# Performance work log

Measured on AMD Instinct MI355X. Metric: run time of the kernel, lower is better.

The kernel has to match this reference:

```python
import jax, jax.numpy as jnp
import numpy as np

G = 9.8          # gravity constant from the module
B = 1024         # buckets per mid layer == spigots per bucket
M = 14           # number of homogeneous mid layers
L = M + 2        # total network layers (head bucket + mids + outlet layer)


def _solve_bucket(H0, S_b, theta_b, inflow):
    """Faithful port of solve_single_bucket.
    H0: scalar head, S_b: (n_sp, 2) [spigot height, area], theta_b: (n_sp,),
    inflow: scalar. Sequential spigot loop -> lax.scan.
    Note: after the first spigot, H_effective = H0 - cum_q/2 (inflow dropped),
    exactly as in the torch code."""
    def step(carry, x):
        H_eff, cum = carry
        sp_h, sp_a, th = x
        h = jnp.maximum(0.0, H_eff - sp_h)
        q = th * jnp.sqrt(2.0 * G * h) * sp_a
        cum = cum + q
        return (H0 - 0.5 * cum, cum), q
    init = (H0 + inflow, jnp.zeros((), S_b.dtype))
    (_, cum_q), qs = jax.lax.scan(step, init, (S_b[:, 0], S_b[:, 1], theta_b))
    H_final = H0 - cum_q + inflow
    return H_final, qs


def setup_inputs() -> dict:
    key = jax.random.key(0)
    ks = jax.random.split(key, 10)
    H0 = jax.random.uniform(ks[0], (1,), jnp.float32) * 5.0
    H_mid = jax.random.uniform(ks[1], (M, B), jnp.float32) * 5.0
    H_last = jax.random.uniform(ks[2], (B,), jnp.float32) * 5.0
    S0 = jax.random.uniform(ks[3], (1, B, 2), jnp.float32)
    S_mid = jax.random.uniform(ks[4], (M, B, B, 2), jnp.float32)
    S_last = jax.random.uniform(ks[5], (B, 1, 2), jnp.float32)
    theta0 = jax.random.uniform(ks[6], (B,), jnp.float32)
    theta_mid = jax.random.uniform(ks[7], (M, B, B), jnp.float32)
    theta_last = jax.random.uniform(ks[8], (B,), jnp.float32)
    precip = jax.random.uniform(ks[9], (), jnp.float32) * 2.0
    return {"H0": H0, "H_mid": H_mid, "H_last": H_last,
            "S0": S0, "S_mid": S_mid, "S_last": S_last,
            "theta0": theta0, "theta_mid": theta_mid, "theta_last": theta_last,
            "precip": precip}


def reference(H0, H_mid, H_last, S0, S_mid, S_last, theta0, theta_mid, theta_last, precip):
    p_layer = precip / L            # precip_inflow_per_layer ('even')
    p_bucket = p_layer / B          # per-bucket share in B-bucket layers

    # layer 0: single head bucket with B spigots, inflow = precip/L
    H0_new, q0 = _solve_bucket(H0[0], S0[0], theta0, p_layer)
    inflow = q0 + p_bucket          # inflow to each of layer-1's B buckets

    # mid layers: vmap over buckets, scan over layers (sequential dependency)
    def mid_layer(inflow, xs):
        H_l, S_l, th_l = xs         # (B,), (B,B,2), (B,B)
        Hn, q = jax.vmap(_solve_bucket)(H_l, S_l, th_l, inflow)
        return q.sum(axis=0) + p_bucket, Hn
    inflow, H_mid_new = jax.lax.scan(mid_layer, inflow, (H_mid, S_mid, theta_mid))

    # last layer: B buckets with a single outlet spigot each
    H_last_new, q_last = jax.vmap(_solve_bucket)(H_last, S_last, theta_last[:, None], inflow)

    # flat output: new heads of all layers + outlet flows
    return jnp.concatenate([H0_new[None], H_mid_new.reshape(-1), H_last_new, q_last.reshape(-1)])
```

## Files before the change

kernel.cpp:

```cpp
#include <hip/hip_runtime.h>
#include <math.h>

#define TWO_G 19.6f
#define NBLK  256

__device__ __attribute__((aligned(256))) unsigned g_flags[NBLK];

__device__ __forceinline__ float flow_q(float th, float d, float a) {
    return th * sqrtf(TWO_G * d) * a;
}

__device__ __forceinline__ float wave_sum(float v) {
#pragma unroll
    for (int o = 32; o > 0; o >>= 1) v += __shfl_xor(v, o);
    return v;
}

__device__ __forceinline__ float lane_bcast(float v, int j) {
    return __int_as_float(__builtin_amdgcn_readlane(__float_as_int(v), j));
}

__device__ __forceinline__ float ld_agent(const float* p) {
    return __hip_atomic_load(p, __ATOMIC_RELAXED, __HIP_MEMORY_SCOPE_AGENT);
}
__device__ __forceinline__ void st_agent(float* p, float v) {
    __hip_atomic_store(p, v, __ATOMIC_RELAXED, __HIP_MEMORY_SCOPE_AGENT);
}
__device__ __forceinline__ unsigned ld_flag(const unsigned* p) {
    return __hip_atomic_load(p, __ATOMIC_RELAXED, __HIP_MEMORY_SCOPE_AGENT);
}
__device__ __forceinline__ void st_flag(unsigned* p, unsigned v) {
    __hip_atomic_store(p, v, __ATOMIC_RELAXED, __HIP_MEMORY_SCOPE_AGENT);
}

__device__ __forceinline__ void dma16(const void* g, void* l) {
    __builtin_amdgcn_global_load_lds(
        (const __attribute__((address_space(1))) unsigned int*)g,
        (__attribute__((address_space(3))) unsigned int*)l, 16, 0, 0);
}

__device__ __forceinline__ void grid_barrier(unsigned target, int bid, int tid) {
    __syncthreads();
    if (tid < 64) {
        if (tid == 0) st_flag(&g_flags[bid], target);
        for (;;) {
            int ok = 1;
#pragma unroll
            for (int k = 0; k < 4; ++k) {
                unsigned f = ld_flag(&g_flags[k * 64 + tid]);
                ok &= ((int)(f - target) >= 0);
            }
            if (__all(ok)) break;
            __builtin_amdgcn_s_sleep(1);
        }
    }
    __syncthreads();
    asm volatile("" ::: "memory");
}

__device__ __forceinline__ float solve_lds(float H, float inflow, int lane,
                                           const char* buf, float* acc) {
    const float2* Sb = (const float2*)buf;
    const float*  Tb = (const float*)(buf + 8192);

    float2 s_cur = Sb[lane];
    float  t_cur = Tb[lane];

    float h0 = lane_bcast(s_cur.x, 0);
    float a0 = lane_bcast(s_cur.y, 0);
    float t0 = lane_bcast(t_cur, 0);
    float d0 = (H + inflow) - h0;
    float q0 = (d0 > 0.0f) ? flow_q(t0, d0, a0) : 0.0f;
    float cum = q0;
    float u   = H - 0.5f * cum;
    if (lane == 0 && q0 != 0.0f) atomicAdd(&acc[0], q0);

#pragma unroll
    for (int c = 0; c < 16; ++c) {
        float2 s = s_cur;
        float  t = t_cur;
        if (c < 15) {
            s_cur = Sb[(c + 1) * 64 + lane];
            t_cur = Tb[(c + 1) * 64 + lane];
        }
        unsigned long long avail = (c == 0) ? ~1ull : ~0ull;
        unsigned long long cand  = __ballot(s.x < u) & avail;
        float qmine = 0.0f;
        while (cand) {
            int j = __builtin_ctzll(cand);
            float hj = lane_bcast(s.x, j);
            float aj = lane_bcast(s.y, j);
            float tj = lane_bcast(t, j);
            float d = u - hj;
            float q = flow_q(tj, d, aj);
            cum += q;
            u = H - 0.5f * cum;
            if (lane == j) qmine = q;
            if (j >= 63) break;
            avail &= (~0ull << (j + 1));
            cand = __ballot(s.x < u) & avail;
        }
        if (qmine != 0.0f) atomicAdd(&acc[c * 64 + lane], qmine);
    }
    return cum;
}

__device__ __forceinline__ void layer0_body(const float* __restrict__ H0p,
                                            const float* __restrict__ S0,
                                            const float* __restrict__ theta0,
                                            const float* __restrict__ precip,
                                            float* __restrict__ out,
                                            float* __restrict__ P0, int lane) {
    const float H  = H0p[0];
    const float pl = precip[0] * 0.0625f;
    const float2* S2 = (const float2*)S0;
    float2 sv[16]; float tv[16];
#pragma unroll
    for (int c = 0; c < 16; ++c) { sv[c] = S2[c * 64 + lane]; tv[c] = theta0[c * 64 + lane]; }

    float h0 = lane_bcast(sv[0].x, 0);
    float a0 = lane_bcast(sv[0].y, 0);
    float t0 = lane_bcast(tv[0], 0);
    float d0 = (H + pl) - h0;
    float q0 = (d0 > 0.0f) ? flow_q(t0, d0, a0) : 0.0f;
    float cum = q0;
    float u   = H - 0.5f * cum;
    if (lane == 0) st_agent(&P0[0], q0);

#pragma unroll
    for (int c = 0; c < 16; ++c) {
        int i = c * 64 + lane;
        float2 s = sv[c];
        unsigned long long avail = (c == 0) ? ~1ull : ~0ull;
        unsigned long long cand  = __ballot(s.x < u) & avail;
        float qmine = 0.0f;
        while (cand) {
            int j = __builtin_ctzll(cand);
            float hj = lane_bcast(s.x, j);
            float aj = lane_bcast(s.y, j);
            float tj = lane_bcast(tv[c], j);
            float d = u - hj;
            float q = flow_q(tj, d, aj);
            cum += q;
            u = H - 0.5f * cum;
            if (lane == j) qmine = q;
            if (j >= 63) break;
            avail &= (~0ull << (j + 1));
            cand = __ballot(s.x < u) & avail;
        }
        if (i > 0) st_agent(&P0[i], qmine);
    }
    if (lane == 0) out[0] = (H - cum) + pl;
}

__global__ __launch_bounds__(256, 1)
void cascade_kernel(const float* __restrict__ H0p, const float* __restrict__ Hmid,
                    const float* __restrict__ Hlast, const float* __restrict__ S0,
                    const float* __restrict__ Smid, const float* __restrict__ Slast,
                    const float* __restrict__ th0, const float* __restrict__ thmid,
                    const float* __restrict__ thlast, const float* __restrict__ precip,
                    float* __restrict__ out, float* __restrict__ PA, float* __restrict__ PB)
{
    __shared__ float acc[1024];
    __shared__ __align__(16) char sbuf[4][12288];

    const int tid  = threadIdx.x;
    const int lane = tid & 63;
    const int w    = tid >> 6;
    const int bid  = blockIdx.x;
    const int b    = bid * 4 + w;

    const unsigned base = ld_flag(&g_flags[bid]);

#pragma unroll
    for (int r = 0; r < 4; ++r) acc[r * 256 + tid] = 0.0f;

    const float pb = precip[0] * (0.0625f / 1024.0f);

    {
        char* dst = sbuf[w];
        const char* gS = (const char*)Smid + (size_t)b * 8192;
        const char* gT = (const char*)thmid + (size_t)b * 4096;
#pragma unroll
        for (int i = 0; i < 8; ++i) dma16(gS + i * 1024 + lane * 16, dst + i * 1024);
#pragma unroll
        for (int i = 0; i < 4; ++i) dma16(gT + i * 1024 + lane * 16, dst + 8192 + i * 1024);
    }
    if (bid == 0 && w == 0)
        layer0_body(H0p, S0, th0, precip, out, PA, lane);
    asm volatile("s_waitcnt vmcnt(0)" ::: "memory");
    grid_barrier(base + 1u, bid, tid);

#pragma unroll 1
    for (int l = 0; l < 14; ++l) {
        const float* Pin = (l & 1) ? PB : PA;
        float*       Pou = (l & 1) ? PA : PB;

        float part = 0.0f;
        if (l == 0) {
            if (lane == 0) part = ld_agent(&Pin[b]);
        } else {
#pragma unroll
            for (int k = 0; k < 4; ++k)
                part += ld_agent(&Pin[(size_t)(k * 64 + lane) * 1024 + b]);
        }
        const float H      = Hmid[(size_t)l * 1024 + b];
        const float inflow = pb + wave_sum(part);

        const float cum = solve_lds(H, inflow, lane, sbuf[w], acc);
        if (lane == 0) out[1 + (size_t)l * 1024 + b] = (H - cum) + inflow;

        __syncthreads();

#pragma unroll
        for (int r = 0; r < 4; ++r) {
            const int idx = r * 256 + tid;
            st_agent(&Pou[(size_t)bid * 1024 + idx], acc[idx]);
            acc[idx] = 0.0f;
        }
        asm volatile("" ::: "memory");

        if (l < 13) {
            char* dst = sbuf[w];
            const char* gS = (const char*)Smid + (size_t)(l + 1) * 8388608 + (size_t)b * 8192;
            const char* gT = (const char*)thmid + (size_t)(l + 1) * 4194304 + (size_t)b * 4096;
#pragma unroll
            for (int i = 0; i < 8; ++i) dma16(gS + i * 1024 + lane * 16, dst + i * 1024);
#pragma unroll
            for (int i = 0; i < 4; ++i) dma16(gT + i * 1024 + lane * 16, dst + 8192 + i * 1024);
            asm volatile("s_waitcnt vmcnt(12)" ::: "memory");
        } else {
            asm volatile("s_waitcnt vmcnt(0)" ::: "memory");
        }

        grid_barrier(base + 2u + (unsigned)l, bid, tid);
        asm volatile("s_waitcnt vmcnt(0)" ::: "memory");
    }

    {
        float part = 0.0f;
#pragma unroll
        for (int k = 0; k < 4; ++k)
            part += ld_agent(&PA[(size_t)(k * 64 + lane) * 1024 + b]);
        const float inflow = pb + wave_sum(part);
        if (lane == 0) {
            const float  Hv = Hlast[b];
            const float2 s  = ((const float2*)Slast)[b];
            const float  d  = (Hv + inflow) - s.x;
            const float  q  = (d > 0.0f) ? flow_q(thlast[b], d, s.y) : 0.0f;
            out[1 + 14 * 1024 + b]        = (Hv - q) + inflow;
            out[1 + 14 * 1024 + 1024 + b] = q;
        }
    }
}

extern "C" void kernel_launch(void* const* d_in, const int* in_sizes, int n_in,
                              void* d_out, int out_size, void* d_ws, size_t ws_size,
                              hipStream_t stream)
{
    (void)in_sizes; (void)n_in; (void)out_size; (void)ws_size;
    const float* H0     = (const float*)d_in[0];
    const float* Hmid   = (const float*)d_in[1];
    const float* Hlast  = (const float*)d_in[2];
    const float* S0     = (const float*)d_in[3];
    const float* Smid   = (const float*)d_in[4];
    const float* Slast  = (const float*)d_in[5];
    const float* th0    = (const float*)d_in[6];
    const float* thmid  = (const float*)d_in[7];
    const float* thlast = (const float*)d_in[8];
    const float* precip = (const float*)d_in[9];
    float* out = (float*)d_out;
    float* PA  = (float*)d_ws;
    float* PB  = PA + (size_t)256 * 1024;

    cascade_kernel<<<dim3(256), dim3(256), 0, stream>>>(
        H0, Hmid, Hlast, S0, Smid, Slast, th0, thmid, thlast, precip, out, PA, PB);
}
```

Baseline: 334.6 us.

## Vectorize cross-block partial-sum gather via dwordx4 loads and LDS transpose

Each thread now loads one 16-byte vector of partial flows from the inter-layer buffer instead of four scattered scalar agent-scope loads, then transposes through a small LDS array so each wave can sum its bucket's partials. This cuts the number of global memory transactions on the latency-critical path between grid barriers, at the cost of an extra __syncthreads and an inline-asm load that waits for all outstanding loads. It also swaps sqrtf for the raw hardware sqrt builtin and simplifies the spigot-mask update to drop a branch. The vmcnt(0) inside the asm load also drains the pending prefetch DMA, which may serialize it with the next layer's compute.

Result: no change. 328.8 us (-1.7%).

```diff
diff --git a/kernel.cpp b/kernel.cpp
--- a/kernel.cpp
+++ b/kernel.cpp
@@ -4,10 +4,12 @@
 #define TWO_G 19.6f
 #define NBLK  256
 
+typedef __attribute__((ext_vector_type(4))) float f32x4;
+
 __device__ __attribute__((aligned(256))) unsigned g_flags[NBLK];
 
 __device__ __forceinline__ float flow_q(float th, float d, float a) {
-    return th * sqrtf(TWO_G * d) * a;
+    return th * __builtin_amdgcn_sqrtf(TWO_G * d) * a;
 }
 
 __device__ __forceinline__ float wave_sum(float v) {
@@ -31,6 +33,14 @@
 }
 __device__ __forceinline__ void st_flag(unsigned* p, unsigned v) {
     __hip_atomic_store(p, v, __ATOMIC_RELAXED, __HIP_MEMORY_SCOPE_AGENT);
+}
+
+__device__ __forceinline__ f32x4 ld_agent4(const float* p) {
+    f32x4 r;
+    asm volatile("global_load_dwordx4 %0, %1, off sc1\n\t"
+                 "s_waitcnt vmcnt(0)"
+                 : "=v"(r) : "v"(p) : "memory");
+    return r;
 }
 
 __device__ __forceinline__ void dma16(const void* g, void* l) {
@@ -96,8 +106,7 @@
             cum += q;
             u = H - 0.5f * cum;
             if (lane == j) qmine = q;
-            if (j >= 63) break;
-            avail &= (~0ull << (j + 1));
+            avail &= (~1ull) << j;
             cand = __ballot(s.x < u) & avail;
         }
         if (qmine != 0.0f) atomicAdd(&acc[c * 64 + lane], qmine);
@@ -144,8 +153,7 @@
             cum += q;
             u = H - 0.5f * cum;
             if (lane == j) qmine = q;
-            if (j >= 63) break;
-            avail &= (~0ull << (j + 1));
+            avail &= (~1ull) << j;
             cand = __ballot(s.x < u) & avail;
         }
         if (i > 0) st_agent(&P0[i], qmine);
@@ -163,6 +171,7 @@
 {
     __shared__ float acc[1024];
     __shared__ __align__(16) char sbuf[4][12288];
+    __shared__ float xpose[256][5];
 
     const int tid  = threadIdx.x;
     const int lane = tid & 63;
@@ -200,9 +209,12 @@
         if (l == 0) {
             if (lane == 0) part = ld_agent(&Pin[b]);
         } else {
-#pragma unroll
-            for (int k = 0; k < 4; ++k)
-                part += ld_agent(&Pin[(size_t)(k * 64 + lane) * 1024 + b]);
+            f32x4 v = ld_agent4(Pin + (size_t)tid * 1024 + bid * 4);
+            xpose[tid][0] = v.x; xpose[tid][1] = v.y;
+            xpose[tid][2] = v.z; xpose[tid][3] = v.w;
+            __syncthreads();
+#pragma unroll
+            for (int r = 0; r < 4; ++r) part += xpose[r * 64 + lane][w];
         }
         const float H      = Hmid[(size_t)l * 1024 + b];
         const float inflow = pb + wave_sum(part);
@@ -238,10 +250,13 @@
     }
 
     {
+        f32x4 v = ld_agent4(PA + (size_t)tid * 1024 + bid * 4);
+        xpose[tid][0] = v.x; xpose[tid][1] = v.y;
+        xpose[tid][2] = v.z; xpose[tid][3] = v.w;
+        __syncthreads();
         float part = 0.0f;
 #pragma unroll
-        for (int k = 0; k < 4; ++k)
-            part += ld_agent(&PA[(size_t)(k * 64 + lane) * 1024 + b]);
+        for (int r = 0; r < 4; ++r) part += xpose[r * 64 + lane][w];
         const float inflow = pb + wave_sum(part);
         if (lane == 0) {
             const float  Hv = Hlast[b];
```
